# Performance work log

Hardware: AMD Instinct MI355X
Metric: run time of the kernel (lower is better)

Reference implementation:

```python
import jax, jax.numpy as jnp
import numpy as np

B, S, H, R = 64, 2048, 512, 256
NEG = -1.0e9


def setup_inputs() -> dict:
    key = jax.random.key(0)
    ks = jax.random.split(key, 12)
    sc_h = 1.0 / np.sqrt(H)
    sc_r = 1.0 / np.sqrt(R)
    return {
        "sent_h": jax.random.normal(ks[0], (B, S, H), jnp.float32),
        "rel": jax.random.normal(ks[1], (B, R), jnp.float32),
        "pool": jax.random.normal(ks[2], (B, H), jnp.float32),
        "mask": jax.random.randint(ks[3], (B, S), 0, 2, jnp.int32),
        "Wg_w": jax.random.normal(ks[4], (H, H), jnp.float32) * sc_h,
        "Wg_b": jnp.zeros((H,), jnp.float32),
        "Wh_w": jax.random.normal(ks[5], (H, H), jnp.float32) * sc_h,
        "Wh_b": jnp.zeros((H,), jnp.float32),
        "Wr_w": jax.random.normal(ks[6], (H, R), jnp.float32) * sc_r,
        "Wr_b": jnp.zeros((H,), jnp.float32),
        "alpha_w": jax.random.normal(ks[7], (1, H), jnp.float32) * sc_h,
        "alpha_b": jnp.zeros((1,), jnp.float32),
    }


def reference(sent_h, rel, pool, mask, Wg_w, Wg_b, Wh_w, Wh_b, Wr_w, Wr_b, alpha_w, alpha_b):
    # linear projections (torch Linear: x @ W.T + b)
    relation = rel @ Wr_w.T + Wr_b          # [B, H]
    sent = jnp.einsum('bsh,kh->bsk', sent_h, Wh_w) + Wh_b  # [B, S, H]
    global_sen = pool @ Wg_w.T + Wg_b       # [B, H]
    mix = jnp.tanh(relation[:, None, :] + sent + global_sen[:, None, :])  # [B, S, H]
    weight = jnp.einsum('bsh,h->bs', mix, alpha_w[0]) + alpha_b[0]        # [B, S]
    weight = jnp.where(mask == 0, NEG, weight)
    weight_ = jax.nn.softmax(weight, axis=-1)
    att_res = jnp.einsum('bs,bsh->bh', weight_, sent)  # [B, H]
    return (att_res, weight_)
```

## Files before the change

### kernel.cpp

```cpp
#include <hip/hip_runtime.h>
#include <cstdint>
#include <cstddef>

#define B_ 64
#define S_ 2048
#define H_ 512
#define R_ 256
#define M_ (B_ * S_)
#define NEGV (-1.0e9f)

typedef short short8 __attribute__((ext_vector_type(8)));
typedef unsigned short u16x8 __attribute__((ext_vector_type(8)));
typedef float f32x4 __attribute__((ext_vector_type(4)));
typedef unsigned short u16;

__device__ __forceinline__ u16 f2b(float x) {
    union { float f; uint32_t u; } c; c.f = x;
    uint32_t u = c.u;
    uint32_t r = (u + 0x7fffu + ((u >> 16) & 1u)) >> 16;
    return (u16)r;
}
__device__ __forceinline__ float b2f(u16 u) {
    union { uint32_t u; float f; } c; c.u = ((uint32_t)u) << 16;
    return c.f;
}
__device__ __forceinline__ uint32_t pk2(float lo, float hi) {
    uint32_t r;
    asm("v_cvt_pk_bf16_f32 %0, %1, %2" : "=v"(r) : "v"(lo), "v"(hi));
    return r;
}
__device__ __forceinline__ void load_lds16(const void* g, void* l) {
    __builtin_amdgcn_global_load_lds((__attribute__((address_space(1))) void*)g,
                                     (__attribute__((address_space(3))) void*)l,
                                     16, 0, 0);
}

__global__ void k_base(const float* __restrict__ rel, const float* __restrict__ pool,
                       const float* __restrict__ Wg_w, const float* __restrict__ Wg_b,
                       const float* __restrict__ Wh_b,
                       const float* __restrict__ Wr_w, const float* __restrict__ Wr_b,
                       const float* __restrict__ whw, float* __restrict__ base,
                       u16* __restrict__ whwb) {
    int tid = threadIdx.x;
    {
        int gi = blockIdx.x * 256 + tid;
        float4 v = ((const float4*)whw)[gi];
        ushort4 o; o.x = f2b(v.x); o.y = f2b(v.y); o.z = f2b(v.z); o.w = f2b(v.w);
        ((ushort4*)whwb)[gi] = o;
    }
    int b = blockIdx.x >> 2, q = blockIdx.x & 3;
    __shared__ __attribute__((aligned(16))) float srel[R_];
    __shared__ __attribute__((aligned(16))) float spool[H_];
    __shared__ float accs[128];
    srel[tid & 255] = rel[b * R_ + (tid & 255)];
    for (int i = tid; i < H_; i += 256) spool[i] = pool[b * H_ + i];
    __syncthreads();
    int kk = tid & 127, half = tid >> 7;
    int k = q * 128 + kk;
    float acc = 0.f;
    if (half == 0) {
        acc = Wr_b[k] + Wg_b[k] + Wh_b[k];
        const float4* wr = (const float4*)(Wr_w + (size_t)k * R_);
        #pragma unroll 8
        for (int r4 = 0; r4 < R_ / 4; ++r4) {
            float4 w = wr[r4]; float4 x = ((const float4*)srel)[r4];
            acc += w.x * x.x + w.y * x.y + w.z * x.z + w.w * x.w;
        }
        const float4* wg = (const float4*)(Wg_w + (size_t)k * H_);
        #pragma unroll 8
        for (int h4 = 0; h4 < 32; ++h4) {
            float4 w = wg[h4]; float4 x = ((const float4*)spool)[h4];
            acc += w.x * x.x + w.y * x.y + w.z * x.z + w.w * x.w;
        }
    } else {
        const float4* wg = (const float4*)(Wg_w + (size_t)k * H_);
        #pragma unroll 8
        for (int h4 = 32; h4 < 128; ++h4) {
            float4 w = wg[h4]; float4 x = ((const float4*)spool)[h4];
            acc += w.x * x.x + w.y * x.y + w.z * x.z + w.w * x.w;
        }
    }
    if (half) accs[kk] = acc;
    __syncthreads();
    if (!half) base[b * H_ + k] = acc + accs[kk];
}

__launch_bounds__(256)
__global__ void k_gemm(const float* __restrict__ A32,
                       const u16* __restrict__ Bw,
                       const float* __restrict__ base,
                       const float* __restrict__ alpha,
                       float* __restrict__ partial)
{
    const int K = 512;
    int j = blockIdx.x;
    int xcd  = j & 7;
    int slot = j >> 3;
    int nb   = slot & 3;
    int mb   = (slot >> 2) * 8 + xcd;
    int m0 = mb * 128;
    int n0 = nb * 128;
    int b  = m0 >> 11;

    int tid = threadIdx.x;
    int w  = tid >> 6;
    int l  = tid & 63;
    int wm = w & 1, wn = w >> 1;
    int lr = l & 15;
    int lq = l >> 4;

    __shared__ __attribute__((aligned(16))) u16 smA[2][128 * 64];
    __shared__ __attribute__((aligned(16))) u16 smB[2][128 * 64];
    __shared__ float red[2][2][64];

    f32x4 zero = {0.f, 0.f, 0.f, 0.f};
    f32x4 acc[4][4];
    #pragma unroll
    for (int i = 0; i < 4; ++i)
        #pragma unroll
        for (int jj = 0; jj < 4; ++jj) acc[i][jj] = zero;

    int arow[4], acolg[4];
    #pragma unroll
    for (int i = 0; i < 4; ++i) {
        int c = w * 4 + i;
        arow[i]  = (c >> 1) * 16 + lr;
        acolg[i] = (c & 1) * 32 + lq * 8;
    }

    float4 av[4][2];

    auto LOAD_A = [&](int kt) {
        int k0 = kt * 64;
        #pragma unroll
        for (int i = 0; i < 4; ++i) {
            const float4* ga = (const float4*)(A32 + (size_t)(m0 + arow[i]) * K + k0 + acolg[i]);
            av[i][0] = ga[0];
            av[i][1] = ga[1];
        }
    };
    auto WRITE_A = [&](int buf) {
        #pragma unroll
        for (int i = 0; i < 4; ++i) {
            uint4 pv;
            pv.x = pk2(av[i][0].x, av[i][0].y);
            pv.y = pk2(av[i][0].z, av[i][0].w);
            pv.z = pk2(av[i][1].x, av[i][1].y);
            pv.w = pk2(av[i][1].z, av[i][1].w);
            *(uint4*)(smA[buf] + (w * 4 + i) * 512 + l * 8) = pv;
        }
    };
    auto STAGE_B = [&](int buf, int kt) {
        int k0 = kt * 64;
        #pragma unroll
        for (int i = 0; i < 4; ++i) {
            int c  = w * 4 + i;
            int mf = c >> 1, kc = c & 1;
            int row = mf * 16 + lr;
            int col = k0 + kc * 32 + lq * 8;
            const u16* gb = Bw + (size_t)(n0 + row) * K + col;
            load_lds16(gb, smB[buf] + c * 512);
        }
    };

    LOAD_A(0);
    STAGE_B(0, 0);
    WRITE_A(0);
    __syncthreads();

    #pragma unroll
    for (int kt = 0; kt < 8; ++kt) {
        int cur = kt & 1;
        if (kt < 7) {
            LOAD_A(kt + 1);
            STAGE_B(cur ^ 1, kt + 1);
        }
        __builtin_amdgcn_s_setprio(1);
        #pragma unroll
        for (int kc = 0; kc < 2; ++kc) {
            short8 af[4], bf[4];
            #pragma unroll
            for (int mi = 0; mi < 4; ++mi)
                af[mi] = *(const short8*)(smA[cur] + ((wm * 4 + mi) * 2 + kc) * 512 + l * 8);
            #pragma unroll
            for (int ni = 0; ni < 4; ++ni)
                bf[ni] = *(const short8*)(smB[cur] + ((wn * 4 + ni) * 2 + kc) * 512 + l * 8);
            #pragma unroll
            for (int mi = 0; mi < 4; ++mi)
                #pragma unroll
                for (int ni = 0; ni < 4; ++ni)
                    acc[mi][ni] = __builtin_amdgcn_mfma_f32_16x16x32_bf16(af[mi], bf[ni], acc[mi][ni], 0, 0, 0);
        }
        __builtin_amdgcn_s_setprio(0);
        if (kt < 7) WRITE_A(cur ^ 1);
        __syncthreads();
    }

    const float C2 = 2.8853900817779268f;
    float base2[4], a2[4];
    float asum = 0.f;
    #pragma unroll
    for (int ni = 0; ni < 4; ++ni) {
        int n = n0 + wn * 64 + ni * 16 + lr;
        base2[ni] = C2 * base[b * H_ + n];
        float al  = alpha[n];
        a2[ni] = 2.0f * al;
        asum  += al;
    }
    #pragma unroll
    for (int mi = 0; mi < 4; ++mi) {
        #pragma unroll
        for (int r = 0; r < 4; ++r) {
            float s = asum;
            #pragma unroll
            for (int ni = 0; ni < 4; ++ni) {
                float f  = fmaf(acc[mi][ni][r], C2, base2[ni]);
                float e  = __builtin_amdgcn_exp2f(f);
                float rr = __builtin_amdgcn_rcpf(e + 1.0f);
                s = fmaf(-a2[ni], rr, s);
            }
            s += __shfl_xor(s, 1);
            s += __shfl_xor(s, 2);
            s += __shfl_xor(s, 4);
            s += __shfl_xor(s, 8);
            if (lr == 0) red[wm][wn][mi * 16 + lq * 4 + r] = s;
        }
    }
    __syncthreads();
    if (tid < 128) {
        int wmi = tid >> 6, row = tid & 63;
        float sum = red[wmi][0][row] + red[wmi][1][row];
        partial[(size_t)nb * M_ + m0 + wmi * 64 + row] = sum;
    }
}

__global__ void k_softmax(const float* __restrict__ partial, const int* __restrict__ mask,
                          const float* __restrict__ alpha_b, float* __restrict__ wout) {
    int b = blockIdx.x;
    int tid = threadIdx.x;
    __shared__ float sred[8];
    float x[8];
    float ab = alpha_b[0];
    float lmax = -3.0e38f;
    #pragma unroll
    for (int jj = 0; jj < 8; ++jj) {
        int s = tid + jj * 256;
        size_t m = (size_t)b * S_ + s;
        float v = partial[m] + partial[(size_t)M_ + m] + partial[2 * (size_t)M_ + m] + partial[3 * (size_t)M_ + m] + ab;
        if (mask[b * S_ + s] == 0) v = NEGV;
        x[jj] = v;
        lmax = fmaxf(lmax, v);
    }
    #pragma unroll
    for (int off = 1; off < 64; off <<= 1) lmax = fmaxf(lmax, __shfl_xor(lmax, off));
    int wv = tid >> 6, l = tid & 63;
    if (l == 0) sred[wv] = lmax;
    __syncthreads();
    float gmax = fmaxf(fmaxf(sred[0], sred[1]), fmaxf(sred[2], sred[3]));
    float lsum = 0.f;
    #pragma unroll
    for (int jj = 0; jj < 8; ++jj) { x[jj] = __expf(x[jj] - gmax); lsum += x[jj]; }
    #pragma unroll
    for (int off = 1; off < 64; off <<= 1) lsum += __shfl_xor(lsum, off);
    if (l == 0) sred[4 + wv] = lsum;
    __syncthreads();
    float inv = 1.f / (sred[4] + sred[5] + sred[6] + sred[7]);
    #pragma unroll
    for (int jj = 0; jj < 8; ++jj) {
        int s = tid + jj * 256;
        wout[(size_t)b * S_ + s] = x[jj] * inv;
    }
}

__global__ void k_wsum(const float* __restrict__ sent, const float* __restrict__ wrow_g,
                       float* __restrict__ t) {
    int b  = blockIdx.x >> 3;
    int hc = blockIdx.x & 7;
    int tid = threadIdx.x;
    __shared__ __attribute__((aligned(16))) float wrow[S_];
    __shared__ float red[64][33];
    ((float4*)wrow)[tid]       = ((const float4*)(wrow_g + (size_t)b * S_))[tid];
    ((float4*)wrow)[tid + 256] = ((const float4*)(wrow_g + (size_t)b * S_))[tid + 256];
    __syncthreads();
    int hi = tid & 7;
    int sg = tid >> 3;
    const float* bp = sent + (size_t)b * S_ * H_ + hc * 64 + hi * 8;
    float acc[8] = {0.f, 0.f, 0.f, 0.f, 0.f, 0.f, 0.f, 0.f};
    for (int sb = 0; sb < S_; sb += 256) {
        float4 v[8][2];
        #pragma unroll
        for (int u = 0; u < 8; ++u) {
            const float4* p = (const float4*)(bp + (size_t)(sb + sg + u * 32) * H_);
            v[u][0] = p[0]; v[u][1] = p[1];
        }
        #pragma unroll
        for (int u = 0; u < 8; ++u) {
            float wgt = wrow[sb + sg + u * 32];
            acc[0] = fmaf(wgt, v[u][0].x, acc[0]);
            acc[1] = fmaf(wgt, v[u][0].y, acc[1]);
            acc[2] = fmaf(wgt, v[u][0].z, acc[2]);
            acc[3] = fmaf(wgt, v[u][0].w, acc[3]);
            acc[4] = fmaf(wgt, v[u][1].x, acc[4]);
            acc[5] = fmaf(wgt, v[u][1].y, acc[5]);
            acc[6] = fmaf(wgt, v[u][1].z, acc[6]);
            acc[7] = fmaf(wgt, v[u][1].w, acc[7]);
        }
    }
    #pragma unroll
    for (int e = 0; e < 8; ++e) red[hi * 8 + e][sg] = acc[e];
    __syncthreads();
    if (tid < 64) {
        float s = 0.f;
        #pragma unroll
        for (int g = 0; g < 32; ++g) s += red[tid][g];
        t[(size_t)b * H_ + hc * 64 + tid] = s;
    }
}

__global__ void k_att(const float* __restrict__ t, const float* __restrict__ Whw,
                      const float* __restrict__ Whb, float* __restrict__ out) {
    int tid = threadIdx.x;
    int b = blockIdx.x >> 2, q = blockIdx.x & 3;
    __shared__ __attribute__((aligned(16))) float st[H_];
    __shared__ float accs[128];
    for (int i = tid; i < H_; i += 256) st[i] = t[(size_t)b * H_ + i];
    __syncthreads();
    int hh = tid & 127, half = tid >> 7;
    int h = q * 128 + hh;
    const float4* wr = (const float4*)(Whw + (size_t)h * H_) + half * 64;
    const float4* sx = (const float4*)st + half * 64;
    float acc = 0.f;
    #pragma unroll 8
    for (int i = 0; i < 64; ++i) {
        float4 w = wr[i]; float4 x = sx[i];
        acc += w.x * x.x + w.y * x.y + w.z * x.z + w.w * x.w;
    }
    if (half) accs[hh] = acc;
    __syncthreads();
    if (!half) out[(size_t)b * H_ + h] = acc + accs[hh] + Whb[h];
}

extern "C" void kernel_launch(void* const* d_in, const int* in_sizes, int n_in,
                              void* d_out, int out_size, void* d_ws, size_t ws_size,
                              hipStream_t stream) {
    const float* sent_h  = (const float*)d_in[0];
    const float* rel     = (const float*)d_in[1];
    const float* pool    = (const float*)d_in[2];
    const int*   mask    = (const int*)d_in[3];
    const float* Wg_w    = (const float*)d_in[4];
    const float* Wg_b    = (const float*)d_in[5];
    const float* Wh_w    = (const float*)d_in[6];
    const float* Wh_b    = (const float*)d_in[7];
    const float* Wr_w    = (const float*)d_in[8];
    const float* Wr_b    = (const float*)d_in[9];
    const float* alpha_w = (const float*)d_in[10];
    const float* alpha_b = (const float*)d_in[11];
    float* out = (float*)d_out;

    char* ws = (char*)d_ws;
    u16*   whwb    = (u16*)ws;
    float* base    = (float*)(ws + 524288);
    float* partial = (float*)(ws + 524288 + 131072);
    float* tbuf    = (float*)(ws + 524288 + 131072 + 2097152);

    float* att_out = out;
    float* w_out   = out + B_ * H_;

    k_base<<<dim3(256), dim3(256), 0, stream>>>(rel, pool, Wg_w, Wg_b, Wh_b, Wr_w, Wr_b, Wh_w, base, whwb);
    k_gemm<<<dim3((M_ / 128) * 4), dim3(256), 0, stream>>>(sent_h, whwb, base, alpha_w, partial);
    k_softmax<<<dim3(B_), dim3(256), 0, stream>>>(partial, mask, alpha_b, w_out);
    k_wsum<<<dim3(B_ * 8), dim3(256), 0, stream>>>(sent_h, w_out, tbuf);
    k_att<<<dim3(256), dim3(256), 0, stream>>>(tbuf, Wh_w, Wh_b, att_out);
}
```

Before: 578.6 us.

## Load B fragments directly to registers and deepen A/B prefetch to two stages

The B (weight) operand is no longer staged through LDS via global_load_lds. Each wave instead loads its own B MFMA fragments straight into registers from global memory, which removes the smB buffer and its LDS reads. A and B global loads are now double-buffered in registers with a prefetch distance of two k-tiles. The per-iteration __syncthreads is replaced by an explicit lgkmcnt wait plus s_barrier placed at the loop top. This costs more VGPRs and duplicates B reads across the two wm waves, which may hurt occupancy or L2 traffic in exchange for better latency hiding.

```diff
diff --git a/kernel.cpp b/kernel.cpp
--- a/kernel.cpp
+++ b/kernel.cpp
@@ -28,11 +28,6 @@
     uint32_t r;
     asm("v_cvt_pk_bf16_f32 %0, %1, %2" : "=v"(r) : "v"(lo), "v"(hi));
     return r;
-}
-__device__ __forceinline__ void load_lds16(const void* g, void* l) {
-    __builtin_amdgcn_global_load_lds((__attribute__((address_space(1))) void*)g,
-                                     (__attribute__((address_space(3))) void*)l,
-                                     16, 0, 0);
 }
 
 __global__ void k_base(const float* __restrict__ rel, const float* __restrict__ pool,
@@ -95,9 +90,9 @@
     const int K = 512;
     int j = blockIdx.x;
     int xcd  = j & 7;
-    int slot = j >> 3;
-    int nb   = slot & 3;
-    int mb   = (slot >> 2) * 8 + xcd;
+    int slot0 = j >> 3;
+    int nb   = slot0 & 3;
+    int mb   = (slot0 >> 2) * 8 + xcd;
     int m0 = mb * 128;
     int n0 = nb * 128;
     int b  = m0 >> 11;
@@ -110,7 +105,6 @@
     int lq = l >> 4;
 
     __shared__ __attribute__((aligned(16))) u16 smA[2][128 * 64];
-    __shared__ __attribute__((aligned(16))) u16 smB[2][128 * 64];
     __shared__ float red[2][2][64];
 
     f32x4 zero = {0.f, 0.f, 0.f, 0.f};
@@ -120,80 +114,72 @@
         #pragma unroll
         for (int jj = 0; jj < 4; ++jj) acc[i][jj] = zero;
 
-    int arow[4], acolg[4];
+    const float4* gA[4];
     #pragma unroll
     for (int i = 0; i < 4; ++i) {
         int c = w * 4 + i;
-        arow[i]  = (c >> 1) * 16 + lr;
-        acolg[i] = (c & 1) * 32 + lq * 8;
-    }
-
-    float4 av[4][2];
-
-    auto LOAD_A = [&](int kt) {
-        int k0 = kt * 64;
+        gA[i] = (const float4*)(A32 + (size_t)(m0 + (c >> 1) * 16 + lr) * K + (c & 1) * 32 + lq * 8);
+    }
+    const short8* gB[4];
+    #pragma unroll
+    for (int ni = 0; ni < 4; ++ni)
+        gB[ni] = (const short8*)(Bw + (size_t)(n0 + wn * 64 + ni * 16 + lr) * K + lq * 8);
+
+    float4 av[2][4][2];
+    short8 bv[2][2][4];
+
+    auto LOAD_A = [&](int slot, int kt) {
         #pragma unroll
         for (int i = 0; i < 4; ++i) {
-            const float4* ga = (const float4*)(A32 + (size_t)(m0 + arow[i]) * K + k0 + acolg[i]);
-            av[i][0] = ga[0];
-            av[i][1] = ga[1];
+            av[slot][i][0] = gA[i][kt * 16];
+            av[slot][i][1] = gA[i][kt * 16 + 1];
         }
     };
-    auto WRITE_A = [&](int buf) {
+    auto LOAD_B = [&](int slot, int kt) {
+        #pragma unroll
+        for (int kc = 0; kc < 2; ++kc)
+            #pragma unroll
+            for (int ni = 0; ni < 4; ++ni)
+                bv[slot][kc][ni] = gB[ni][kt * 8 + kc * 4];
+    };
+    auto WRITE_A = [&](int buf, int slot) {
         #pragma unroll
         for (int i = 0; i < 4; ++i) {
             uint4 pv;
-            pv.x = pk2(av[i][0].x, av[i][0].y);
-            pv.y = pk2(av[i][0].z, av[i][0].w);
-            pv.z = pk2(av[i][1].x, av[i][1].y);
-            pv.w = pk2(av[i][1].z, av[i][1].w);
+            pv.x = pk2(av[slot][i][0].x, av[slot][i][0].y);
+            pv.y = pk2(av[slot][i][0].z, av[slot][i][0].w);
+            pv.z = pk2(av[slot][i][1].x, av[slot][i][1].y);
+            pv.w = pk2(av[slot][i][1].z, av[slot][i][1].w);
             *(uint4*)(smA[buf] + (w * 4 + i) * 512 + l * 8) = pv;
         }
     };
-    auto STAGE_B = [&](int buf, int kt) {
-        int k0 = kt * 64;
-        #pragma unroll
-        for (int i = 0; i < 4; ++i) {
-            int c  = w * 4 + i;
-            int mf = c >> 1, kc = c & 1;
-            int row = mf * 16 + lr;
-            int col = k0 + kc * 32 + lq * 8;
-            const u16* gb = Bw + (size_t)(n0 + row) * K + col;
-            load_lds16(gb, smB[buf] + c * 512);
-        }
-    };
-
-    LOAD_A(0);
-    STAGE_B(0, 0);
-    WRITE_A(0);
-    __syncthreads();
+
+    LOAD_A(0, 0); LOAD_B(0, 0);
+    LOAD_A(1, 1); LOAD_B(1, 1);
+    WRITE_A(0, 0);
 
     #pragma unroll
     for (int kt = 0; kt < 8; ++kt) {
-        int cur = kt & 1;
-        if (kt < 7) {
-            LOAD_A(kt + 1);
-            STAGE_B(cur ^ 1, kt + 1);
-        }
+        const int cur = kt & 1, nxt = cur ^ 1, slot = kt & 1;
+        asm volatile("s_waitcnt lgkmcnt(0)" ::: "memory");
+        __builtin_amdgcn_s_barrier();
+        __builtin_amdgcn_sched_barrier(0);
         __builtin_amdgcn_s_setprio(1);
         #pragma unroll
         for (int kc = 0; kc < 2; ++kc) {
-            short8 af[4], bf[4];
+            short8 af[4];
             #pragma unroll
             for (int mi = 0; mi < 4; ++mi)
                 af[mi] = *(const short8*)(smA[cur] + ((wm * 4 + mi) * 2 + kc) * 512 + l * 8);
             #pragma unroll
-            for (int ni = 0; ni < 4; ++ni)
-                bf[ni] = *(const short8*)(smB[cur] + ((wn * 4 + ni) * 2 + kc) * 512 + l * 8);
-            #pragma unroll
             for (int mi = 0; mi < 4; ++mi)
                 #pragma unroll
                 for (int ni = 0; ni < 4; ++ni)
-                    acc[mi][ni] = __builtin_amdgcn_mfma_f32_16x16x32_bf16(af[mi], bf[ni], acc[mi][ni], 0, 0, 0);
+                    acc[mi][ni] = __builtin_amdgcn_mfma_f32_16x16x32_bf16(af[mi], bv[slot][kc][ni], acc[mi][ni], 0, 0, 0);
         }
         __builtin_amdgcn_s_setprio(0);
-        if (kt < 7) WRITE_A(cur ^ 1);
-        __syncthreads();
+        if (kt < 6) { LOAD_A(slot, kt + 2); LOAD_B(slot, kt + 2); }
+        if (kt < 7) WRITE_A(nxt, (kt + 1) & 1);
     }
 
     const float C2 = 2.8853900817779268f;
@@ -207,6 +193,7 @@
         a2[ni] = 2.0f * al;
         asum  += al;
     }
+    __syncthreads();
     #pragma unroll
     for (int mi = 0; mi < 4; ++mi) {
         #pragma unroll
```

New measurement: 587.9 us. Within noise of the previous version (+1.6%).
